# Kernel optimization log

Measured on AMD Instinct MI355X. Metric: run time of the kernel, lower is better.

Reference implementation:

```python
import jax, jax.numpy as jnp
import numpy as np

B, T, C = 4, 2048, 1024
E = 8            # n_expert
K = 2            # n_expert_per_token
H = 1408         # moe_intermediate_size
HS = 1408 * 2    # shared expert intermediate (moe_intermediate_size * n_shared_expert)


def setup_inputs() -> dict:
    key = jax.random.key(0)
    k = jax.random.split(key, 8)
    s = 0.02
    return {
        "x":   jax.random.normal(k[0], (B, T, C), jnp.float32),
        "Wg":  jax.random.normal(k[1], (C, E), jnp.float32) * s,      # router gate
        "W1":  jax.random.normal(k[2], (E, C, H), jnp.float32) * s,   # fc_1 per expert
        "W2":  jax.random.normal(k[3], (E, C, H), jnp.float32) * s,   # fc_2 per expert
        "W3":  jax.random.normal(k[4], (E, H, C), jnp.float32) * s,   # proj per expert
        "Ws1": jax.random.normal(k[5], (C, HS), jnp.float32) * s,     # shared fc_1
        "Ws2": jax.random.normal(k[6], (C, HS), jnp.float32) * s,     # shared fc_2
        "Ws3": jax.random.normal(k[7], (HS, C), jnp.float32) * s,     # shared proj
    }


def reference(x, Wg, W1, W2, W3, Ws1, Ws2, Ws3):
    b, t, c = x.shape
    xf = x.reshape(-1, c)                       # [N, C]
    n = xf.shape[0]

    # Router: top-k then softmax over the selected logits (float32 softmax).
    router = xf @ Wg                            # [N, E]
    top_logits, idx = jax.lax.top_k(router, K)  # [N, K]
    probs = jax.nn.softmax(top_logits.astype(jnp.float32), axis=-1).astype(x.dtype)

    # token_expert_weights: scatter probs into dense [N, E] per-expert weights.
    w = jnp.zeros((n, E), x.dtype).at[jnp.arange(n)[:, None], idx].add(probs)

    # Per-expert gated MLP on all tokens; zero-weight tokens contribute nothing,
    # matching the masked gather/scatter-add of the original.
    h = jax.nn.silu(jnp.einsum('tc,ech->eth', xf, W1)) * jnp.einsum('tc,ech->eth', xf, W2)
    y = jnp.einsum('eth,ehc,te->tc', h, W3, w)  # weighted combine
    y = y.reshape(b, t, c)

    # Shared expert on the residual input.
    hs = jax.nn.silu(xf @ Ws1) * (xf @ Ws2)     # [N, HS]
    y = y + (hs @ Ws3).reshape(b, t, c)
    return y
```

## Files before the change

### kernel.cpp

```cpp
#include <hip/hip_runtime.h>
#include <cstdint>

#define NTOK 8192
#define CDIM 1024
#define HDIM 1408
#define HSDIM 2816
#define NEXP 8

typedef __attribute__((ext_vector_type(8))) short s8v;
typedef __attribute__((ext_vector_type(4))) float f4v;
typedef __attribute__((ext_vector_type(8))) unsigned short u16x8;

__device__ __forceinline__ unsigned short f2bf(float f) {
    unsigned int u = __float_as_uint(f);
    unsigned int r = (u + 0x7fffu + ((u >> 16) & 1u)) >> 16;
    return (unsigned short)r;
}
__device__ __forceinline__ float bf2f(unsigned short u) {
    return __uint_as_float(((unsigned int)u) << 16);
}


__global__ void cvt_bf16_kernel(const float4* __restrict__ in, ushort4* __restrict__ out, int n4) {
    int i = blockIdx.x * blockDim.x + threadIdx.x;
    if (i < n4) {
        float4 v = in[i];
        ushort4 o;
        o.x = f2bf(v.x); o.y = f2bf(v.y); o.z = f2bf(v.z); o.w = f2bf(v.w);
        out[i] = o;
    }
}

__global__ __launch_bounds__(256) void transpose_cvt_kernel(
    const float* __restrict__ in0, const float* __restrict__ in1,
    unsigned short* __restrict__ out0, unsigned short* __restrict__ out1,
    int R, int Cc, int zsplit) {
    __shared__ float T[64][68];
    int z = blockIdx.z;
    const float* in = (z < zsplit) ? in0 : in1;
    unsigned short* out = (z < zsplit) ? out0 : out1;
    int zz = (z < zsplit) ? z : z - zsplit;
    const size_t bs = (size_t)R * Cc;
    in += zz * bs; out += zz * bs;

    const int t = threadIdx.x;
    const int r0 = blockIdx.y * 64, c0 = blockIdx.x * 64;

    {
        const int rl = t >> 2, cq = t & 3;
        const float* src = in + (size_t)(r0 + rl) * Cc + c0;
#pragma unroll
        for (int i = 0; i < 4; i++) {
            float4 v = *(const float4*)(src + (cq + 4 * i) * 4);
            *(float4*)&T[rl][(cq + 4 * i) * 4] = v;
        }
    }
    __syncthreads();
    {
        const int cl = t >> 2, rq = t & 3;
        unsigned short* dst = out + (size_t)(c0 + cl) * R + r0 + rq * 16;
        u16x8 lo, hi;
#pragma unroll
        for (int j = 0; j < 8; j++) lo[j] = f2bf(T[rq * 16 + j][cl]);
#pragma unroll
        for (int j = 0; j < 8; j++) hi[j] = f2bf(T[rq * 16 + 8 + j][cl]);
        *(u16x8*)dst = lo;
        *(u16x8*)(dst + 8) = hi;
    }
}

__global__ void router_kernel(const float* __restrict__ x, const float* __restrict__ Wg,
                              int* __restrict__ idxK, float* __restrict__ probK,
                              int* __restrict__ meta) {
    int t = blockIdx.x;
    int lane = threadIdx.x;
    const float* xr = x + (size_t)t * CDIM;
    float acc[NEXP];
#pragma unroll
    for (int e = 0; e < NEXP; e++) acc[e] = 0.f;
    for (int c = lane; c < CDIM; c += 64) {
        float xv = xr[c];
        const float* wr = Wg + c * NEXP;
#pragma unroll
        for (int e = 0; e < NEXP; e++) acc[e] += xv * wr[e];
    }
#pragma unroll
    for (int e = 0; e < NEXP; e++)
        for (int off = 32; off > 0; off >>= 1)
            acc[e] += __shfl_down(acc[e], off, 64);
    if (lane == 0) {
        int b0 = 0; float v0 = acc[0];
#pragma unroll
        for (int e = 1; e < NEXP; e++) if (acc[e] > v0) { v0 = acc[e]; b0 = e; }
        int b1 = -1; float v1 = -1e30f;
#pragma unroll
        for (int e = 0; e < NEXP; e++) if (e != b0 && acc[e] > v1) { v1 = acc[e]; b1 = e; }
        float p0 = 1.f / (1.f + __expf(v1 - v0));
        idxK[2 * t] = b0; idxK[2 * t + 1] = b1;
        probK[2 * t] = p0; probK[2 * t + 1] = 1.f - p0;
        atomicAdd(&meta[b0], 1);
        atomicAdd(&meta[b1], 1);
    }
}

__global__ void offsets_kernel(int* meta) {
    int s = 0;
    for (int e = 0; e < NEXP; e++) { meta[8 + e] = s; meta[16 + e] = s; s += meta[e]; }
}

__global__ void fill_kernel(const int* __restrict__ idxK, const float* __restrict__ probK,
                            int* __restrict__ meta, int* __restrict__ rowT, float* __restrict__ rowW,
                            int* __restrict__ tokSlot) {
    int t = blockIdx.x * 256 + threadIdx.x;
    if (t >= NTOK) return;
#pragma unroll
    for (int k = 0; k < 2; k++) {
        int e = idxK[2 * t + k];
        int p = atomicAdd(&meta[16 + e], 1);
        rowT[p] = t;
        rowW[p] = probK[2 * t + k];
        tokSlot[2 * t + k] = p;
    }
}

__global__ __launch_bounds__(256) void gemm12_kernel(
    const unsigned short* __restrict__ xb,
    const unsigned short* __restrict__ w1, const unsigned short* __restrict__ w2,
    const unsigned short* __restrict__ ws1, const unsigned short* __restrict__ ws2,
    unsigned short* __restrict__ hE, unsigned short* __restrict__ hS,
    const int* __restrict__ rowT, const int* __restrict__ meta) {
    const int id = blockIdx.x;
    int z, m0, n0; bool SH;
    if (id < 3520) { SH = false; z = id & 7; int q = id >> 3; m0 = (q % 20) * 128; n0 = (q / 20) * 64; }
    else           { SH = true;  z = 8; int q = id - 3520; m0 = (q & 63) * 128; n0 = (q >> 6) * 64; }
    const int M = SH ? NTOK : meta[z];
    const int base = SH ? 0 : meta[8 + z];
    if (m0 >= M) return;

    const unsigned short* B1 = SH ? ws1 : w1 + (size_t)z * HDIM * CDIM;
    const unsigned short* B2 = SH ? ws2 : w2 + (size_t)z * HDIM * CDIM;

    __shared__ unsigned short L[16384];

    const int tid = threadIdx.x;
    const int srow = tid >> 2;
    const int key = (tid >> 3) & 3;
    const int co = ((tid & 3) ^ key) << 3;

    int am0 = m0 + srow;       am0 = am0 < M ? am0 : M - 1;
    int am1 = m0 + 64 + srow;  am1 = am1 < M ? am1 : M - 1;
    long ar0 = SH ? am0 : rowT[base + am0];
    long ar1 = SH ? am1 : rowT[base + am1];
    const unsigned short* a0p = xb + (size_t)ar0 * CDIM + co;
    const unsigned short* a1p = xb + (size_t)ar1 * CDIM + co;
    const unsigned short* b1p = B1 + (size_t)(n0 + srow) * CDIM + co;
    const unsigned short* b2p = B2 + (size_t)(n0 + srow) * CDIM + co;

    const int w = tid >> 6, lane = tid & 63;
    const int wm = (w >> 1) * 64, wn = (w & 1) * 32;
    const int quad = lane >> 4, l15 = lane & 15;
    const int rcx = (quad ^ ((l15 >> 1) & 3)) << 3;

    f4v acc1[4][2], acc2[4][2];
#pragma unroll
    for (int i = 0; i < 4; i++)
#pragma unroll
        for (int j = 0; j < 2; j++) {
            f4v zz = {0.f, 0.f, 0.f, 0.f};
            acc1[i][j] = zz; acc2[i][j] = zz;
        }

    uint4 r0a0, r0a1, r0b1, r0b2;
    uint4 r1a0, r1a1, r1b1, r1b2;

#define LOADSET12(s, k0) do { \
        r##s##a0 = *(const uint4*)(a0p + (k0)); \
        r##s##a1 = *(const uint4*)(a1p + (k0)); \
        r##s##b1 = *(const uint4*)(b1p + (k0)); \
        r##s##b2 = *(const uint4*)(b2p + (k0)); } while (0)
#define WRITESET12(b, s) do { \
        *(uint4*)(L + (b) * 4096 + tid * 8) = r##s##a0; \
        *(uint4*)(L + (b) * 4096 + 2048 + tid * 8) = r##s##a1; \
        *(uint4*)(L + 8192 + (b) * 2048 + tid * 8) = r##s##b1; \
        *(uint4*)(L + 12288 + (b) * 2048 + tid * 8) = r##s##b2; } while (0)

    auto compute = [&](int b) {
        const unsigned short* Ab = L + b * 4096;
        const unsigned short* B1b = L + 8192 + b * 2048;
        const unsigned short* B2b = L + 12288 + b * 2048;
        s8v af[4], bf1[2], bf2[2];
#pragma unroll
        for (int mt = 0; mt < 4; mt++)
            af[mt] = *(const s8v*)(Ab + (wm + mt * 16 + l15) * 32 + rcx);
#pragma unroll
        for (int nt = 0; nt < 2; nt++) {
            bf1[nt] = *(const s8v*)(B1b + (wn + nt * 16 + l15) * 32 + rcx);
            bf2[nt] = *(const s8v*)(B2b + (wn + nt * 16 + l15) * 32 + rcx);
        }
#pragma unroll
        for (int mt = 0; mt < 4; mt++)
#pragma unroll
            for (int nt = 0; nt < 2; nt++) {
                acc1[mt][nt] = __builtin_amdgcn_mfma_f32_16x16x32_bf16(af[mt], bf1[nt], acc1[mt][nt], 0, 0, 0);
                acc2[mt][nt] = __builtin_amdgcn_mfma_f32_16x16x32_bf16(af[mt], bf2[nt], acc2[mt][nt], 0, 0, 0);
            }
    };

    const int NS = CDIM / 32;
    LOADSET12(0, 0);
    LOADSET12(1, 32);
    WRITESET12(0, 0);
    __syncthreads();
#pragma unroll 1
    for (int ks = 0; ks < NS; ks += 2) {
        if (ks + 2 < NS) LOADSET12(0, (ks + 2) * 32);
        WRITESET12(1, 1);
        compute(0);
        __syncthreads();
        if (ks + 3 < NS) LOADSET12(1, (ks + 3) * 32);
        compute(1);
        WRITESET12(0, 0);
        __syncthreads();
    }
#undef LOADSET12
#undef WRITESET12

#pragma unroll
    for (int mt = 0; mt < 4; mt++) {
#pragma unroll
        for (int r = 0; r < 4; r++) {
            int gm = m0 + wm + mt * 16 + quad * 4 + r;
            if (gm < M) {
                unsigned short* hrow = SH ? hS + (size_t)gm * HSDIM
                                          : hE + (size_t)(base + gm) * HDIM;
#pragma unroll
                for (int nt = 0; nt < 2; nt++) {
                    float z1 = acc1[mt][nt][r];
                    float z2 = acc2[mt][nt][r];
                    float hv = (z1 / (1.f + __expf(-z1))) * z2;
                    hrow[n0 + wn + nt * 16 + l15] = f2bf(hv);
                }
            }
        }
    }
}

__global__ __launch_bounds__(256) void gemm3_kernel(
    const unsigned short* __restrict__ hE, const unsigned short* __restrict__ hS,
    const unsigned short* __restrict__ w3, const unsigned short* __restrict__ ws3,
    float* __restrict__ Out, unsigned short* __restrict__ pE,
    const int* __restrict__ rowT, const float* __restrict__ rowW, const int* __restrict__ meta) {
    const int id = blockIdx.x;
    int z, m0, n0; bool SH;
    if (id < 1280) { SH = false; z = id & 7; int q = id >> 3; m0 = (q % 20) * 128; n0 = (q / 20) * 128; }
    else           { SH = true;  z = 8; int q = id - 1280; m0 = (q & 63) * 128; n0 = (q >> 6) * 128; }
    const int M = SH ? NTOK : meta[z];
    const int base = SH ? 0 : meta[8 + z];
    if (m0 >= M) return;
    const int K = SH ? HSDIM : HDIM;
    const unsigned short* A = SH ? hS : hE;
    const unsigned short* B = SH ? ws3 : w3 + (size_t)z * CDIM * HDIM;

    __shared__ unsigned short L[16384];

    const int tid = threadIdx.x;
    const int srow = tid >> 2;
    const int key = (tid >> 3) & 3;
    const int co = ((tid & 3) ^ key) << 3;

    int am0 = m0 + srow;       am0 = am0 < M ? am0 : M - 1;
    int am1 = m0 + 64 + srow;  am1 = am1 < M ? am1 : M - 1;
    const unsigned short* a0p = A + (size_t)(base + am0) * K + co;
    const unsigned short* a1p = A + (size_t)(base + am1) * K + co;
    const unsigned short* b0p = B + (size_t)(n0 + srow) * K + co;
    const unsigned short* b1p = B + (size_t)(n0 + 64 + srow) * K + co;

    const int w = tid >> 6, lane = tid & 63;
    const int wm = (w >> 1) * 64, wn = (w & 1) * 64;
    const int quad = lane >> 4, l15 = lane & 15;
    const int rcx = (quad ^ ((l15 >> 1) & 3)) << 3;

    f4v acc[4][4];
#pragma unroll
    for (int i = 0; i < 4; i++)
#pragma unroll
        for (int j = 0; j < 4; j++) {
            f4v zz = {0.f, 0.f, 0.f, 0.f};
            acc[i][j] = zz;
        }

    uint4 r0a0, r0a1, r0b0, r0b1;
    uint4 r1a0, r1a1, r1b0, r1b1;

#define LOADSET3(s, k0) do { \
        r##s##a0 = *(const uint4*)(a0p + (k0)); \
        r##s##a1 = *(const uint4*)(a1p + (k0)); \
        r##s##b0 = *(const uint4*)(b0p + (k0)); \
        r##s##b1 = *(const uint4*)(b1p + (k0)); } while (0)
#define WRITESET3(b, s) do { \
        *(uint4*)(L + (b) * 4096 + tid * 8) = r##s##a0; \
        *(uint4*)(L + (b) * 4096 + 2048 + tid * 8) = r##s##a1; \
        *(uint4*)(L + 8192 + (b) * 4096 + tid * 8) = r##s##b0; \
        *(uint4*)(L + 8192 + (b) * 4096 + 2048 + tid * 8) = r##s##b1; } while (0)

    auto compute = [&](int b) {
        const unsigned short* Ab = L + b * 4096;
        const unsigned short* Bb = L + 8192 + b * 4096;
        s8v af[4], bf[4];
#pragma unroll
        for (int mt = 0; mt < 4; mt++)
            af[mt] = *(const s8v*)(Ab + (wm + mt * 16 + l15) * 32 + rcx);
#pragma unroll
        for (int nt = 0; nt < 4; nt++)
            bf[nt] = *(const s8v*)(Bb + (wn + nt * 16 + l15) * 32 + rcx);
#pragma unroll
        for (int mt = 0; mt < 4; mt++)
#pragma unroll
            for (int nt = 0; nt < 4; nt++)
                acc[mt][nt] = __builtin_amdgcn_mfma_f32_16x16x32_bf16(af[mt], bf[nt], acc[mt][nt], 0, 0, 0);
    };

    const int NS = K / 32;
    LOADSET3(0, 0);
    LOADSET3(1, 32);
    WRITESET3(0, 0);
    __syncthreads();
#pragma unroll 1
    for (int ks = 0; ks < NS; ks += 2) {
        if (ks + 2 < NS) LOADSET3(0, (ks + 2) * 32);
        WRITESET3(1, 1);
        compute(0);
        __syncthreads();
        if (ks + 3 < NS) LOADSET3(1, (ks + 3) * 32);
        compute(1);
        WRITESET3(0, 0);
        __syncthreads();
    }
#undef LOADSET3
#undef WRITESET3

#pragma unroll
    for (int mt = 0; mt < 4; mt++) {
#pragma unroll
        for (int r = 0; r < 4; r++) {
            int gm = m0 + wm + mt * 16 + quad * 4 + r;
            if (gm < M) {
                if (SH) {
                    size_t o = (size_t)gm * CDIM + n0 + wn + l15;
#pragma unroll
                    for (int nt = 0; nt < 4; nt++)
                        Out[o + nt * 16] = acc[mt][nt][r];
                } else {
                    size_t o = (size_t)(base + gm) * CDIM + n0 + wn + l15;
#pragma unroll
                    for (int nt = 0; nt < 4; nt++)
                        pE[o + nt * 16] = f2bf(acc[mt][nt][r]);
                }
            }
        }
    }
}

__global__ __launch_bounds__(256) void combine_kernel(
    float* __restrict__ Out, const unsigned short* __restrict__ pE,
    const int* __restrict__ tokSlot, const float* __restrict__ rowW) {
    const int t = blockIdx.x;
    const int c = threadIdx.x * 4;
    const int s0 = tokSlot[2 * t], s1 = tokSlot[2 * t + 1];
    const float w0 = rowW[s0], w1 = rowW[s1];
    float* op = Out + (size_t)t * CDIM + c;
    float4 o = *(float4*)op;
    ushort4 a = *(const ushort4*)(pE + (size_t)s0 * CDIM + c);
    ushort4 b = *(const ushort4*)(pE + (size_t)s1 * CDIM + c);
    o.x += w0 * bf2f(a.x) + w1 * bf2f(b.x);
    o.y += w0 * bf2f(a.y) + w1 * bf2f(b.y);
    o.z += w0 * bf2f(a.z) + w1 * bf2f(b.z);
    o.w += w0 * bf2f(a.w) + w1 * bf2f(b.w);
    *(float4*)op = o;
}


extern "C" void kernel_launch(void* const* d_in, const int* in_sizes, int n_in,
                              void* d_out, int out_size, void* d_ws, size_t ws_size,
                              hipStream_t stream) {
    const float* x   = (const float*)d_in[0];
    const float* Wg  = (const float*)d_in[1];
    const float* W1  = (const float*)d_in[2];
    const float* W2  = (const float*)d_in[3];
    const float* W3  = (const float*)d_in[4];
    const float* Ws1 = (const float*)d_in[5];
    const float* Ws2 = (const float*)d_in[6];
    const float* Ws3 = (const float*)d_in[7];
    float* out = (float*)d_out;

    char* p = (char*)d_ws;
    auto carve = [&](size_t bytes) {
        char* r = p;
        p += (bytes + 255) & ~(size_t)255;
        return r;
    };
    unsigned short* xb   = (unsigned short*)carve((size_t)NTOK * CDIM * 2);
    unsigned short* w1t  = (unsigned short*)carve((size_t)NEXP * HDIM * CDIM * 2);
    unsigned short* w2t  = (unsigned short*)carve((size_t)NEXP * HDIM * CDIM * 2);
    unsigned short* w3t  = (unsigned short*)carve((size_t)NEXP * CDIM * HDIM * 2);
    unsigned short* ws1t = (unsigned short*)carve((size_t)HSDIM * CDIM * 2);
    unsigned short* ws2t = (unsigned short*)carve((size_t)HSDIM * CDIM * 2);
    unsigned short* ws3t = (unsigned short*)carve((size_t)CDIM * HSDIM * 2);
    unsigned short* hE   = (unsigned short*)carve((size_t)2 * NTOK * HDIM * 2);
    unsigned short* hS   = (unsigned short*)carve((size_t)NTOK * HSDIM * 2);
    int*   idxK   = (int*)carve((size_t)NTOK * 2 * 4);
    float* probK  = (float*)carve((size_t)NTOK * 2 * 4);
    int*   rowT   = (int*)carve((size_t)2 * NTOK * 4);
    float* rowW   = (float*)carve((size_t)2 * NTOK * 4);
    int*   tokSlot= (int*)carve((size_t)2 * NTOK * 4);
    int*   meta   = (int*)carve(256);

    unsigned short* pE = w1t;

    cvt_bf16_kernel<<<(NTOK * CDIM / 4 + 255) / 256, 256, 0, stream>>>(
        (const float4*)x, (ushort4*)xb, NTOK * CDIM / 4);
    transpose_cvt_kernel<<<dim3(HDIM / 64, CDIM / 64, 16), 256, 0, stream>>>(
        W1, W2, w1t, w2t, CDIM, HDIM, 8);
    transpose_cvt_kernel<<<dim3(CDIM / 64, HDIM / 64, 8), 256, 0, stream>>>(
        W3, W3, w3t, w3t, HDIM, CDIM, 8);
    transpose_cvt_kernel<<<dim3(HSDIM / 64, CDIM / 64, 2), 256, 0, stream>>>(
        Ws1, Ws2, ws1t, ws2t, CDIM, HSDIM, 1);
    transpose_cvt_kernel<<<dim3(CDIM / 64, HSDIM / 64, 1), 256, 0, stream>>>(
        Ws3, Ws3, ws3t, ws3t, HSDIM, CDIM, 1);

    hipMemsetAsync(meta, 0, 256, stream);
    router_kernel<<<NTOK, 64, 0, stream>>>(x, Wg, idxK, probK, meta);
    offsets_kernel<<<1, 1, 0, stream>>>(meta);
    fill_kernel<<<NTOK / 256, 256, 0, stream>>>(idxK, probK, meta, rowT, rowW, tokSlot);

    gemm12_kernel<<<3520 + 2816, 256, 0, stream>>>(
        xb, w1t, w2t, ws1t, ws2t, hE, hS, rowT, meta);
    gemm3_kernel<<<1280 + 512, 256, 0, stream>>>(
        hE, hS, w3t, ws3t, out, pE, rowT, rowW, meta);
    combine_kernel<<<NTOK, 256, 0, stream>>>(out, pE, tokSlot, rowW);
}
```

Measured before the change: 935.6 us.

## Stage GEMM tiles via direct global-to-LDS loads instead of register staging

```diff
diff --git a/kernel.cpp b/kernel.cpp
--- a/kernel.cpp
+++ b/kernel.cpp
@@ -18,6 +18,12 @@
 }
 __device__ __forceinline__ float bf2f(unsigned short u) {
     return __uint_as_float(((unsigned int)u) << 16);
+}
+
+__device__ __forceinline__ void gld_lds16(const unsigned short* g, unsigned short* l) {
+    __builtin_amdgcn_global_load_lds(
+        (const __attribute__((address_space(1))) void*)g,
+        (__attribute__((address_space(3))) void*)l, 16, 0, 0);
 }
 
 
@@ -170,19 +176,11 @@
             acc1[i][j] = zz; acc2[i][j] = zz;
         }
 
-    uint4 r0a0, r0a1, r0b1, r0b2;
-    uint4 r1a0, r1a1, r1b1, r1b2;
-
-#define LOADSET12(s, k0) do { \
-        r##s##a0 = *(const uint4*)(a0p + (k0)); \
-        r##s##a1 = *(const uint4*)(a1p + (k0)); \
-        r##s##b1 = *(const uint4*)(b1p + (k0)); \
-        r##s##b2 = *(const uint4*)(b2p + (k0)); } while (0)
-#define WRITESET12(b, s) do { \
-        *(uint4*)(L + (b) * 4096 + tid * 8) = r##s##a0; \
-        *(uint4*)(L + (b) * 4096 + 2048 + tid * 8) = r##s##a1; \
-        *(uint4*)(L + 8192 + (b) * 2048 + tid * 8) = r##s##b1; \
-        *(uint4*)(L + 12288 + (b) * 2048 + tid * 8) = r##s##b2; } while (0)
+#define STAGE12(b, k0) do { \
+        gld_lds16(a0p + (k0), L + (b) * 4096 + tid * 8); \
+        gld_lds16(a1p + (k0), L + (b) * 4096 + 2048 + tid * 8); \
+        gld_lds16(b1p + (k0), L + 8192 + (b) * 2048 + tid * 8); \
+        gld_lds16(b2p + (k0), L + 12288 + (b) * 2048 + tid * 8); } while (0)
 
     auto compute = [&](int b) {
         const unsigned short* Ab = L + b * 4096;
@@ -207,23 +205,15 @@
     };
 
     const int NS = CDIM / 32;
-    LOADSET12(0, 0);
-    LOADSET12(1, 32);
-    WRITESET12(0, 0);
+    STAGE12(0, 0);
     __syncthreads();
 #pragma unroll 1
-    for (int ks = 0; ks < NS; ks += 2) {
-        if (ks + 2 < NS) LOADSET12(0, (ks + 2) * 32);
-        WRITESET12(1, 1);
-        compute(0);
+    for (int ks = 0; ks < NS; ks++) {
+        if (ks + 1 < NS) STAGE12((ks + 1) & 1, (ks + 1) * 32);
+        compute(ks & 1);
         __syncthreads();
-        if (ks + 3 < NS) LOADSET12(1, (ks + 3) * 32);
-        compute(1);
-        WRITESET12(0, 0);
-        __syncthreads();
-    }
-#undef LOADSET12
-#undef WRITESET12
+    }
+#undef STAGE12
 
 #pragma unroll
     for (int mt = 0; mt < 4; mt++) {
@@ -289,19 +279,11 @@
             acc[i][j] = zz;
         }
 
-    uint4 r0a0, r0a1, r0b0, r0b1;
-    uint4 r1a0, r1a1, r1b0, r1b1;
-
-#define LOADSET3(s, k0) do { \
-        r##s##a0 = *(const uint4*)(a0p + (k0)); \
-        r##s##a1 = *(const uint4*)(a1p + (k0)); \
-        r##s##b0 = *(const uint4*)(b0p + (k0)); \
-        r##s##b1 = *(const uint4*)(b1p + (k0)); } while (0)
-#define WRITESET3(b, s) do { \
-        *(uint4*)(L + (b) * 4096 + tid * 8) = r##s##a0; \
-        *(uint4*)(L + (b) * 4096 + 2048 + tid * 8) = r##s##a1; \
-        *(uint4*)(L + 8192 + (b) * 4096 + tid * 8) = r##s##b0; \
-        *(uint4*)(L + 8192 + (b) * 4096 + 2048 + tid * 8) = r##s##b1; } while (0)
+#define STAGE3(b, k0) do { \
+        gld_lds16(a0p + (k0), L + (b) * 4096 + tid * 8); \
+        gld_lds16(a1p + (k0), L + (b) * 4096 + 2048 + tid * 8); \
+        gld_lds16(b0p + (k0), L + 8192 + (b) * 4096 + tid * 8); \
+        gld_lds16(b1p + (k0), L + 8192 + (b) * 4096 + 2048 + tid * 8); } while (0)
 
     auto compute = [&](int b) {
         const unsigned short* Ab = L + b * 4096;
@@ -321,23 +303,15 @@
     };
 
     const int NS = K / 32;
-    LOADSET3(0, 0);
-    LOADSET3(1, 32);
-    WRITESET3(0, 0);
+    STAGE3(0, 0);
     __syncthreads();
 #pragma unroll 1
-    for (int ks = 0; ks < NS; ks += 2) {
-        if (ks + 2 < NS) LOADSET3(0, (ks + 2) * 32);
-        WRITESET3(1, 1);
-        compute(0);
+    for (int ks = 0; ks < NS; ks++) {
+        if (ks + 1 < NS) STAGE3((ks + 1) & 1, (ks + 1) * 32);
+        compute(ks & 1);
         __syncthreads();
-        if (ks + 3 < NS) LOADSET3(1, (ks + 3) * 32);
-        compute(1);
-        WRITESET3(0, 0);
-        __syncthreads();
-    }
-#undef LOADSET3
-#undef WRITESET3
+    }
+#undef STAGE3
 
 #pragma unroll
     for (int mt = 0; mt < 4; mt++) {
```

Result: faster. 869.8 us (-7.0%).
